# Kernel optimization log

Hardware: AMD Instinct MI355X
Metric: run time of the kernel (lower is better)

Reference implementation:

```python
import jax, jax.numpy as jnp
import numpy as np

V = 100000   # vocab (emb_size == stoich_size so all 8 branches index safely)
D = 256      # emb_dimension
S = 128      # stoich_dimension
H = 512      # hidden_size
B = 8192     # batch of skip-gram pairs
K = 32       # negative samples per pair
NUM_REGULAR = 60000  # num_regular_words


def _mlp(x, w1, b1, w2, b2):
    # Sequential(Linear(S,H), ReLU, Linear(H,D))
    return jax.nn.relu(x @ w1 + b1) @ w2 + b2


def setup_inputs() -> dict:
    key = jax.random.key(0)
    k = jax.random.split(key, 14)
    initrange = 1.0 / D
    return {
        "pos_u": jax.random.randint(k[0], (B,), 0, V),
        "pos_v": jax.random.randint(k[1], (B,), 0, V),
        "neg_v": jax.random.randint(k[2], (B, K), 0, V),
        "u_emb": jax.random.uniform(k[3], (V, D), jnp.float32, -initrange, initrange),
        "v_emb": jax.random.normal(k[4], (V, D), jnp.float32) * 0.01,
        "stoich": jax.random.uniform(k[5], (V, S), jnp.float32),
        "tw1": jax.random.normal(k[6], (S, H), jnp.float32) * 0.05,
        "tb1": jnp.zeros((H,), jnp.float32),
        "tw2": jax.random.normal(k[7], (H, D), jnp.float32) * 0.05,
        "tb2": jnp.zeros((D,), jnp.float32),
        "cw1": jax.random.normal(k[8], (S, H), jnp.float32) * 0.05,
        "cb1": jnp.zeros((H,), jnp.float32),
        "cw2": jax.random.normal(k[9], (H, D), jnp.float32) * 0.05,
        "cb2": jnp.zeros((D,), jnp.float32),
    }


def _masked_score(emb_u, emb_v, emb_neg_v, u_mask, v_mask, neg_v_mask):
    # pos: [B]
    pos = jnp.clip(jnp.sum(emb_u * emb_v, axis=1), -10.0, 10.0)
    pos = jnp.where(v_mask, 0.0, -jax.nn.log_sigmoid(pos))
    # neg: [B,K] = bmm(emb_neg_v [B,K,D], emb_u [B,D,1])
    neg = jnp.clip(jnp.einsum("bkd,bd->bk", emb_neg_v, emb_u), -10.0, 10.0)
    ls = jnp.where(neg_v_mask, 0.0, jax.nn.log_sigmoid(-neg))
    neg_score = -jnp.sum(ls, axis=1)
    return jnp.where(u_mask, 0.0, pos + neg_score)


def reference(pos_u, pos_v, neg_v, u_emb, v_emb, stoich,
              tw1, tb1, tw2, tb2, cw1, cb1, cw2, cb2):
    emb_u_w = u_emb[pos_u]                 # [B,D]
    emb_v_w = v_emb[pos_v]                 # [B,D]
    emb_neg_v_w = v_emb[neg_v]             # [B,K,D]
    emb_u_m = _mlp(stoich[pos_u], tw1, tb1, tw2, tb2)       # [B,D]
    emb_v_m = _mlp(stoich[pos_v], cw1, cb1, cw2, cb2)       # [B,D]
    emb_neg_v_m = _mlp(stoich[neg_v], cw1, cb1, cw2, cb2)   # [B,K,D]

    u_pairs = [(emb_u_w, pos_u >= NUM_REGULAR), (emb_u_m, pos_u < NUM_REGULAR)]
    v_pairs = [(emb_v_w, pos_v >= NUM_REGULAR), (emb_v_m, pos_v < NUM_REGULAR)]
    n_pairs = [(emb_neg_v_w, neg_v >= NUM_REGULAR), (emb_neg_v_m, neg_v < NUM_REGULAR)]

    total = jnp.zeros((B,), emb_u_w.dtype)
    for eu, um in u_pairs:
        for ev, vm in v_pairs:
            for env, nm in n_pairs:
                total = total + _masked_score(eu, ev, env, um, vm, nm)
    return jnp.mean(total)
```

## Files before the change

### kernel.cpp

```cpp
#include <hip/hip_runtime.h>
#include <hip/hip_bf16.h>
#include <math.h>

#define V_SIZE 100000
#define D_DIM  256
#define S_DIM  128
#define H_DIM  512
#define B_SIZE 8192
#define K_NEG  32
#define NR     60000
#define NMOD   (V_SIZE - NR)

#define TM     48
#define CBLK   834
#define UBLK   171
#define MC_PAD (CBLK * TM)
#define MU_PAD (UBLK * TM)
#define HPAD   516

typedef __attribute__((ext_vector_type(8))) short bf16x8;
typedef __attribute__((ext_vector_type(8))) unsigned short u16x8;
typedef __attribute__((ext_vector_type(4))) float f32x4;

static __device__ __forceinline__ short f2bf(float f) {
    unsigned u = __builtin_bit_cast(unsigned, f);
    unsigned r = (u + 0x7fffu + ((u >> 16) & 1u)) >> 16;
    return (short)r;
}
static __device__ __forceinline__ float bf2f(unsigned short h) {
    return __builtin_bit_cast(float, ((unsigned)h) << 16);
}


#define N_CONV (MC_PAD * S_DIM / 4)
#define N_XU   (MU_PAD * S_DIM / 4)
#define N_TR   393216

__global__ __launch_bounds__(256) void prep_kernel(
    const float* __restrict__ stoich, const int* __restrict__ pos_u,
    const float* __restrict__ tw1, const float* __restrict__ cw1,
    const float* __restrict__ tw2, const float* __restrict__ cw2,
    short* __restrict__ xc, short* __restrict__ xu,
    short* __restrict__ W1T_t, short* __restrict__ W1T_c,
    short* __restrict__ W2T_t, short* __restrict__ W2T_c)
{
    int t = blockIdx.x * 256 + threadIdx.x;
    if (t < N_CONV + N_XU) {
        const bool cside = t < N_CONV;
        const int e    = (cside ? t : t - N_CONV) * 4;
        const int j0   = e & 7;
        const int lane = (e >> 3) & 63;
        const int ks   = (e >> 9) & 3;
        const int rt   = e >> 11;
        const int row  = rt * 16 + (lane & 15);
        const int k    = ks * 32 + (lane >> 4) * 8 + j0;
        short4 o = {0, 0, 0, 0};
        if (cside) {
            if (row < NMOD) {
                const float4 v = *(const float4*)(stoich + (size_t)(NR + row) * S_DIM + k);
                o.x = f2bf(v.x); o.y = f2bf(v.y); o.z = f2bf(v.z); o.w = f2bf(v.w);
            }
            ((short4*)xc)[t] = o;
        } else {
            if (row < B_SIZE) {
                int pu = pos_u[row];
                const float4 v = *(const float4*)(stoich + (size_t)pu * S_DIM + k);
                o.x = f2bf(v.x); o.y = f2bf(v.y); o.z = f2bf(v.z); o.w = f2bf(v.w);
            }
            ((short4*)xu)[t - N_CONV] = o;
        }
    } else {
        int t3 = t - (N_CONV + N_XU);
        if (t3 < 131072) {
            const float* src = (t3 < 65536) ? tw1 : cw1;
            short*       dst = (t3 < 65536) ? W1T_t : W1T_c;
            int t4 = t3 & 65535;
            int j = t4 & 7, lane = (t4 >> 3) & 63;
            int nt = (t4 >> 9) & 31, ks = (t4 >> 14) & 3;
            int k = ks * 32 + (lane >> 4) * 8 + j, n = nt * 16 + (lane & 15);
            dst[t4] = f2bf(src[(size_t)k * H_DIM + n]);
        } else {
            int t5 = t3 - 131072;
            const float* src = (t5 < 131072) ? tw2 : cw2;
            short*       dst = (t5 < 131072) ? W2T_t : W2T_c;
            int t4 = t5 & 131071;
            int j = t4 & 7, lane = (t4 >> 3) & 63;
            int nt = (t4 >> 9) & 15, ks = (t4 >> 13) & 15;
            int k = ks * 32 + (lane >> 4) * 8 + j, n = nt * 16 + (lane & 15);
            dst[t4] = f2bf(src[(size_t)k * D_DIM + n]);
        }
    }
}

__global__ __launch_bounds__(256, 3) void fused_mlp_kernel(
    const short* __restrict__ Xc,  const short* __restrict__ W1c,
    const float* __restrict__ b1c, const short* __restrict__ W2c,
    const float* __restrict__ b2c, short* __restrict__ outc,
    const short* __restrict__ Xu,  const short* __restrict__ W1u,
    const float* __restrict__ b1u, const short* __restrict__ W2u,
    const float* __restrict__ b2u, short* __restrict__ outu)
{
    __shared__ short sH[TM * HPAD];

    const int blk = blockIdx.x;
    const short *A, *W1T, *W2T; const float *b1, *b2; short* out;
    int m0, rtb;
    if (blk < CBLK) { A = Xc; W1T = W1c; b1 = b1c; W2T = W2c; b2 = b2c;
                      out = outc; m0 = blk * TM; rtb = blk * 3; }
    else            { A = Xu; W1T = W1u; b1 = b1u; W2T = W2u; b2 = b2u;
                      out = outu; m0 = (blk - CBLK) * TM; rtb = (blk - CBLK) * 3; }

    const int lane = threadIdx.x & 63;
    const int wv   = threadIdx.x >> 6;
    const int fr   = lane & 15;
    const int q    = lane >> 4;

    const short* Ap = A + (size_t)rtb * 2048 + lane * 8;
    bf16x8 af[4][3];
    #pragma unroll
    for (int ks = 0; ks < 4; ++ks)
        #pragma unroll
        for (int mi = 0; mi < 3; ++mi)
            af[ks][mi] = *(const bf16x8*)(Ap + mi * 2048 + ks * 512);

    #pragma unroll
    for (int half = 0; half < 2; ++half) {
        const int nt0 = wv * 8 + half * 4;
        const short* Bp = W1T + (size_t)nt0 * 512 + lane * 8;
        f32x4 acc[3][4] = {};
        #pragma unroll
        for (int ks = 0; ks < 4; ++ks) {
            bf16x8 bfr[4];
            #pragma unroll
            for (int ni = 0; ni < 4; ++ni)
                bfr[ni] = *(const bf16x8*)(Bp + ks * 16384 + ni * 512);
            #pragma unroll
            for (int mi = 0; mi < 3; ++mi)
                #pragma unroll
                for (int ni = 0; ni < 4; ++ni)
                    acc[mi][ni] = __builtin_amdgcn_mfma_f32_16x16x32_bf16(
                        af[ks][mi], bfr[ni], acc[mi][ni], 0, 0, 0);
        }
        #pragma unroll
        for (int ni = 0; ni < 4; ++ni) {
            int c = (nt0 + ni) * 16 + fr;
            float bv = b1[c];
            #pragma unroll
            for (int mi = 0; mi < 3; ++mi)
                #pragma unroll
                for (int r = 0; r < 4; ++r)
                    sH[(mi * 16 + q * 4 + r) * HPAD + c] =
                        f2bf(fmaxf(acc[mi][ni][r] + bv, 0.f));
        }
    }

    const short* Bp2 = W2T + (size_t)(wv * 4) * 512 + lane * 8;
    f32x4 acc2[3][4] = {};
    bf16x8 bA[4], bB[4], bC[4], bD[4], aA[3], aB[3];

    #define LOAD_B(ks, dst)                                                   \
        _Pragma("unroll")                                                     \
        for (int ni = 0; ni < 4; ++ni)                                        \
            dst[ni] = *(const bf16x8*)(Bp2 + (ks) * 8192 + ni * 512);
    #define LOAD_A(ks, dst)                                                   \
        _Pragma("unroll")                                                     \
        for (int mi = 0; mi < 3; ++mi) {                                      \
            const short* hp = &sH[(mi * 16 + fr) * HPAD + (ks) * 32 + q * 8]; \
            short4 lo = *(const short4*)hp;                                   \
            short4 hi = *(const short4*)(hp + 4);                             \
            bf16x8 v;                                                         \
            v[0] = lo.x; v[1] = lo.y; v[2] = lo.z; v[3] = lo.w;               \
            v[4] = hi.x; v[5] = hi.y; v[6] = hi.z; v[7] = hi.w;               \
            dst[mi] = v;                                                      \
        }

    LOAD_B(0, bA);
    LOAD_B(1, bB);
    LOAD_B(2, bC);
    __syncthreads();
    LOAD_A(0, aA);
    #pragma unroll
    for (int ks = 0; ks < 16; ++ks) {
        if (ks < 13) { LOAD_B(ks + 3, bD); }
        if (ks < 15) { LOAD_A(ks + 1, aB); }
        #pragma unroll
        for (int mi = 0; mi < 3; ++mi)
            #pragma unroll
            for (int ni = 0; ni < 4; ++ni)
                acc2[mi][ni] = __builtin_amdgcn_mfma_f32_16x16x32_bf16(
                    aA[mi], bA[ni], acc2[mi][ni], 0, 0, 0);
        if (ks < 15) {
            #pragma unroll
            for (int i = 0; i < 4; ++i) { bA[i] = bB[i]; bB[i] = bC[i]; bC[i] = bD[i]; }
            #pragma unroll
            for (int i = 0; i < 3; ++i) aA[i] = aB[i];
        }
    }
    #undef LOAD_A
    #undef LOAD_B

    float bv[4];
    #pragma unroll
    for (int ni = 0; ni < 4; ++ni)
        bv[ni] = b2[wv * 64 + ni * 16 + fr];
    #pragma unroll
    for (int mi = 0; mi < 3; ++mi)
        #pragma unroll
        for (int r = 0; r < 4; ++r) {
            int row = m0 + mi * 16 + q * 4 + r;
            short4 s;
            s.x = f2bf(acc2[mi][0][r] + bv[0]);
            s.y = f2bf(acc2[mi][1][r] + bv[1]);
            s.z = f2bf(acc2[mi][2][r] + bv[2]);
            s.w = f2bf(acc2[mi][3][r] + bv[3]);
            *(short4*)(out + (size_t)row * D_DIM + wv * 64 + fr * 4) = s;
        }
}

__device__ __forceinline__ float logsig_fast(float x) {
    float t = __expf(-fabsf(x));
    return fminf(x, 0.f) - __logf(1.f + t);
}
__device__ __forceinline__ float clip10(float x) {
    return fminf(fmaxf(x, -10.f), 10.f);
}

__global__ __launch_bounds__(256) void score_kernel(
    const int*   __restrict__ pos_u,
    const int*   __restrict__ pos_v,
    const int*   __restrict__ neg_v,
    const float* __restrict__ u_emb,
    const float* __restrict__ v_emb,
    const unsigned short* __restrict__ tab_c,
    const unsigned short* __restrict__ Ubuf,
    float* __restrict__ partials)
{
    const int b    = blockIdx.x;
    const int lane = threadIdx.x & 63;
    const int wv   = threadIdx.x >> 6;
    const int g    = lane >> 4;
    const int l    = lane & 15;
    const int w64  = (l >> 2) * 64;
    const int s4   = (l & 3) * 4;

    float euf[16];
    int pu = pos_u[b];
    if (pu < NR) {
        const float* eup = u_emb + (size_t)pu * D_DIM;
        #pragma unroll
        for (int n = 0; n < 4; ++n) {
            float4 v = *(const float4*)(eup + w64 + n * 16 + s4);
            euf[0 + n] = v.x; euf[4 + n] = v.y; euf[8 + n] = v.z; euf[12 + n] = v.w;
        }
    } else {
        const unsigned short* eup = Ubuf + (size_t)b * D_DIM + l * 16;
        u16x8 h0 = *(const u16x8*)eup;
        u16x8 h1 = *(const u16x8*)(eup + 8);
        #pragma unroll
        for (int i = 0; i < 8; ++i) { euf[i] = bf2f(h0[i]); euf[8 + i] = bf2f(h1[i]); }
    }

    float part = 0.f;
    const int* nv = neg_v + (size_t)b * K_NEG + wv * 8;

    #pragma unroll
    for (int it = 0; it < 3; ++it) {
        int ix;
        if (it < 2)            ix = nv[it * 4 + g];
        else if (wv == 0)      ix = pos_v[b];
        else                   break;
        float d = 0.f;
        if (ix < NR) {
            const float* rp = v_emb + (size_t)ix * D_DIM;
            #pragma unroll
            for (int n = 0; n < 4; ++n) {
                float4 v = *(const float4*)(rp + w64 + n * 16 + s4);
                d += euf[0 + n] * v.x + euf[4 + n] * v.y
                   + euf[8 + n] * v.z + euf[12 + n] * v.w;
            }
        } else {
            const unsigned short* rp = tab_c + (size_t)(ix - NR) * D_DIM + l * 16;
            u16x8 h0 = *(const u16x8*)rp;
            u16x8 h1 = *(const u16x8*)(rp + 8);
            #pragma unroll
            for (int i = 0; i < 8; ++i)
                d += euf[i] * bf2f(h0[i]) + euf[8 + i] * bf2f(h1[i]);
        }
        #pragma unroll
        for (int o = 1; o < 16; o <<= 1) d += __shfl_xor(d, o, 64);
        if (it < 2)        part -= logsig_fast(-clip10(d));
        else if (g == 0)   part -= logsig_fast( clip10(d));
    }

    float ws = part;
    #pragma unroll
    for (int o = 32; o; o >>= 1) ws += __shfl_xor(ws, o, 64);
    __shared__ float sp[4];
    if (lane == 0) sp[wv] = ws * 0.0625f;
    __syncthreads();
    if (threadIdx.x == 0)
        partials[b] = sp[0] + sp[1] + sp[2] + sp[3];
}

__global__ __launch_bounds__(256) void reduce_kernel(
    const float* __restrict__ partials, float* __restrict__ out)
{
    float s = 0.f;
    for (int i = threadIdx.x; i < B_SIZE; i += 256) s += partials[i];
    #pragma unroll
    for (int o = 32; o; o >>= 1) s += __shfl_xor(s, o, 64);
    __shared__ float sp[4];
    if ((threadIdx.x & 63) == 0) sp[threadIdx.x >> 6] = s;
    __syncthreads();
    if (threadIdx.x == 0)
        out[0] = (sp[0] + sp[1] + sp[2] + sp[3]) * (2.0f / (float)B_SIZE);
}

extern "C" void kernel_launch(void* const* d_in, const int* in_sizes, int n_in,
                              void* d_out, int out_size, void* d_ws, size_t ws_size,
                              hipStream_t stream) {
    const int*   pos_u  = (const int*)  d_in[0];
    const int*   pos_v  = (const int*)  d_in[1];
    const int*   neg_v  = (const int*)  d_in[2];
    const float* u_emb  = (const float*)d_in[3];
    const float* v_emb  = (const float*)d_in[4];
    const float* stoich = (const float*)d_in[5];
    const float* tw1    = (const float*)d_in[6];
    const float* tb1    = (const float*)d_in[7];
    const float* tw2    = (const float*)d_in[8];
    const float* tb2    = (const float*)d_in[9];
    const float* cw1    = (const float*)d_in[10];
    const float* cb1    = (const float*)d_in[11];
    const float* cw2    = (const float*)d_in[12];
    const float* cb2    = (const float*)d_in[13];
    float* out = (float*)d_out;

    char* ws = (char*)d_ws;
    short* Xbf   = (short*)(ws);
    short* Xu    = (short*)(ws + 10248192);
    short* W1T_t = (short*)(ws + 12349440);
    short* W1T_c = (short*)(ws + 12480512);
    short* W2T_t = (short*)(ws + 12611584);
    short* W2T_c = (short*)(ws + 12873728);
    short* tab_c = (short*)(ws + 13135872);
    short* Ubuf  = (short*)(ws + 33632256);
    float* parts = (float*)(ws + 37834752);

    dim3 blk(256);

    prep_kernel<<<dim3((N_CONV + N_XU + N_TR) / 256), blk, 0, stream>>>(
        stoich, pos_u, tw1, cw1, tw2, cw2,
        Xbf, Xu, W1T_t, W1T_c, W2T_t, W2T_c);

    fused_mlp_kernel<<<dim3(CBLK + UBLK), blk, 0, stream>>>(
        Xbf, W1T_c, cb1, W2T_c, cb2, tab_c,
        Xu,  W1T_t, tb1, W2T_t, tb2, Ubuf);

    score_kernel<<<dim3(B_SIZE), blk, 0, stream>>>(
        pos_u, pos_v, neg_v, u_emb, v_emb,
        (const unsigned short*)tab_c, (const unsigned short*)Ubuf, parts);
    reduce_kernel<<<dim3(1), blk, 0, stream>>>(parts, out);
}
```

Baseline: 290.8 us.

## Unify v-side table into one bf16 buffer and hoist gathers before compute

The prep kernel now converts the first NR rows of v_emb to bf16 in a layout matching the score kernel's per-lane 16-element slices, and the MLP writes its outputs directly after them, forming one contiguous v table. The score kernel drops the per-index branch between fp32 v_emb and the bf16 MLP table, issuing all row gathers up front so their loads overlap. This cuts gather bytes and divergence in the score kernel, but adds a full read and write pass over 60000x256 floats in prep, and the v embeddings for regular words are rounded to bf16.

```diff
diff --git a/kernel.cpp b/kernel.cpp
--- a/kernel.cpp
+++ b/kernel.cpp
@@ -32,19 +32,33 @@
 }
 
 
+#define N_VC   (NR * D_DIM / 4)
 #define N_CONV (MC_PAD * S_DIM / 4)
 #define N_XU   (MU_PAD * S_DIM / 4)
 #define N_TR   393216
 
 __global__ __launch_bounds__(256) void prep_kernel(
     const float* __restrict__ stoich, const int* __restrict__ pos_u,
+    const float* __restrict__ v_emb,
     const float* __restrict__ tw1, const float* __restrict__ cw1,
     const float* __restrict__ tw2, const float* __restrict__ cw2,
+    short* __restrict__ vall,
     short* __restrict__ xc, short* __restrict__ xu,
     short* __restrict__ W1T_t, short* __restrict__ W1T_c,
     short* __restrict__ W2T_t, short* __restrict__ W2T_c)
 {
     int t = blockIdx.x * 256 + threadIdx.x;
+    if (t < N_VC) {
+        int r  = t >> 6;
+        int fr = t & 15;
+        int wv = (t & 63) >> 4;
+        const float* rp = v_emb + (size_t)r * D_DIM + wv * 64 + fr;
+        short4 o;
+        o.x = f2bf(rp[0]); o.y = f2bf(rp[16]); o.z = f2bf(rp[32]); o.w = f2bf(rp[48]);
+        ((short4*)vall)[t] = o;
+        return;
+    }
+    t -= N_VC;
     if (t < N_CONV + N_XU) {
         const bool cside = t < N_CONV;
         const int e    = (cside ? t : t - N_CONV) * 4;
@@ -230,8 +244,7 @@
     const int*   __restrict__ pos_v,
     const int*   __restrict__ neg_v,
     const float* __restrict__ u_emb,
-    const float* __restrict__ v_emb,
-    const unsigned short* __restrict__ tab_c,
+    const unsigned short* __restrict__ Vall,
     const unsigned short* __restrict__ Ubuf,
     float* __restrict__ partials)
 {
@@ -243,6 +256,22 @@
     const int w64  = (l >> 2) * 64;
     const int s4   = (l & 3) * 4;
 
+    const int* nv = neg_v + (size_t)b * K_NEG + wv * 8;
+    int ix0 = nv[g];
+    int ix1 = nv[4 + g];
+    const unsigned short* r0p = Vall + (size_t)ix0 * D_DIM + l * 16;
+    const unsigned short* r1p = Vall + (size_t)ix1 * D_DIM + l * 16;
+    u16x8 r0a = *(const u16x8*)r0p;
+    u16x8 r0b = *(const u16x8*)(r0p + 8);
+    u16x8 r1a = *(const u16x8*)r1p;
+    u16x8 r1b = *(const u16x8*)(r1p + 8);
+    u16x8 rpa, rpb;
+    if (wv == 0) {
+        const unsigned short* rpp = Vall + (size_t)pos_v[b] * D_DIM + l * 16;
+        rpa = *(const u16x8*)rpp;
+        rpb = *(const u16x8*)(rpp + 8);
+    }
+
     float euf[16];
     int pu = pos_u[b];
     if (pu < NR) {
@@ -261,35 +290,29 @@
     }
 
     float part = 0.f;
-    const int* nv = neg_v + (size_t)b * K_NEG + wv * 8;
-
-    #pragma unroll
-    for (int it = 0; it < 3; ++it) {
-        int ix;
-        if (it < 2)            ix = nv[it * 4 + g];
-        else if (wv == 0)      ix = pos_v[b];
-        else                   break;
-        float d = 0.f;
-        if (ix < NR) {
-            const float* rp = v_emb + (size_t)ix * D_DIM;
-            #pragma unroll
-            for (int n = 0; n < 4; ++n) {
-                float4 v = *(const float4*)(rp + w64 + n * 16 + s4);
-                d += euf[0 + n] * v.x + euf[4 + n] * v.y
-                   + euf[8 + n] * v.z + euf[12 + n] * v.w;
-            }
-        } else {
-            const unsigned short* rp = tab_c + (size_t)(ix - NR) * D_DIM + l * 16;
-            u16x8 h0 = *(const u16x8*)rp;
-            u16x8 h1 = *(const u16x8*)(rp + 8);
-            #pragma unroll
-            for (int i = 0; i < 8; ++i)
-                d += euf[i] * bf2f(h0[i]) + euf[8 + i] * bf2f(h1[i]);
-        }
-        #pragma unroll
-        for (int o = 1; o < 16; o <<= 1) d += __shfl_xor(d, o, 64);
-        if (it < 2)        part -= logsig_fast(-clip10(d));
-        else if (g == 0)   part -= logsig_fast( clip10(d));
+
+    float d0 = 0.f, d1 = 0.f;
+    #pragma unroll
+    for (int i = 0; i < 8; ++i) {
+        d0 += euf[i] * bf2f(r0a[i]) + euf[8 + i] * bf2f(r0b[i]);
+        d1 += euf[i] * bf2f(r1a[i]) + euf[8 + i] * bf2f(r1b[i]);
+    }
+    #pragma unroll
+    for (int o = 1; o < 16; o <<= 1) {
+        d0 += __shfl_xor(d0, o, 64);
+        d1 += __shfl_xor(d1, o, 64);
+    }
+    part -= logsig_fast(-clip10(d0));
+    part -= logsig_fast(-clip10(d1));
+
+    if (wv == 0) {
+        float dp = 0.f;
+        #pragma unroll
+        for (int i = 0; i < 8; ++i)
+            dp += euf[i] * bf2f(rpa[i]) + euf[8 + i] * bf2f(rpb[i]);
+        #pragma unroll
+        for (int o = 1; o < 16; o <<= 1) dp += __shfl_xor(dp, o, 64);
+        if (g == 0) part -= logsig_fast(clip10(dp));
     }
 
     float ws = part;
@@ -342,22 +365,23 @@
     short* W1T_c = (short*)(ws + 12480512);
     short* W2T_t = (short*)(ws + 12611584);
     short* W2T_c = (short*)(ws + 12873728);
-    short* tab_c = (short*)(ws + 13135872);
-    short* Ubuf  = (short*)(ws + 33632256);
-    float* parts = (float*)(ws + 37834752);
+    short* Vall  = (short*)(ws + 13135872);
+    short* Ubuf  = (short*)(ws + 64352256);
+    float* parts = (float*)(ws + 68554752);
+    short* tab_c = Vall + (size_t)NR * D_DIM;
 
     dim3 blk(256);
 
-    prep_kernel<<<dim3((N_CONV + N_XU + N_TR) / 256), blk, 0, stream>>>(
-        stoich, pos_u, tw1, cw1, tw2, cw2,
-        Xbf, Xu, W1T_t, W1T_c, W2T_t, W2T_c);
+    prep_kernel<<<dim3((N_VC + N_CONV + N_XU + N_TR) / 256), blk, 0, stream>>>(
+        stoich, pos_u, v_emb, tw1, cw1, tw2, cw2,
+        Vall, Xbf, Xu, W1T_t, W1T_c, W2T_t, W2T_c);
 
     fused_mlp_kernel<<<dim3(CBLK + UBLK), blk, 0, stream>>>(
         Xbf, W1T_c, cb1, W2T_c, cb2, tab_c,
         Xu,  W1T_t, tb1, W2T_t, tb2, Ubuf);
 
     score_kernel<<<dim3(B_SIZE), blk, 0, stream>>>(
-        pos_u, pos_v, neg_v, u_emb, v_emb,
-        (const unsigned short*)tab_c, (const unsigned short*)Ubuf, parts);
+        pos_u, pos_v, neg_v, u_emb,
+        (const unsigned short*)Vall, (const unsigned short*)Ubuf, parts);
     reduce_kernel<<<dim3(1), blk, 0, stream>>>(parts, out);
 }
```

Measured after the change: 291.7 us. About the same (+0.3%).
